# Optimization experiments

Hardware: AMD Instinct MI355X
Metric: run time of the kernel (lower is better)

Reference implementation:

```python
import jax, jax.numpy as jnp
import numpy as np

N_HEADS = 2
N_POINTS = 3
BN_EPS = 1e-5


def make_pe(C, D):
    # PositionalEncoding buffer, sliced to depth D: shape (D, C)
    pos = np.arange(D, dtype=np.float32)[:, None]
    div = np.exp(np.arange(0, C, 2, dtype=np.float32) * (-np.log(10000.0) / C))
    pe = np.zeros((D, C), dtype=np.float32)
    pe[:, 0::2] = np.sin(pos * div)
    pe[:, 1::2] = np.cos(pos * div)
    return jnp.asarray(pe)


def setup_inputs() -> dict:
    key = jax.random.key(0)
    b, c, zs, h, w = 2, 256, 32, 48, 48
    hp = N_HEADS * N_POINTS
    ks = jax.random.split(key, 8)
    features = jax.random.normal(ks[0], (b, c, zs, h, w), dtype=jnp.float32)
    # 1x1 Conv3d weights (out_ch, in_ch), no bias
    q_w = jax.random.normal(ks[1], (c, c), dtype=jnp.float32) * 0.05
    v_w = jax.random.normal(ks[2], (c, c), dtype=jnp.float32) * 0.05
    o_w = jax.random.normal(ks[3], (c, c), dtype=jnp.float32) * 0.05
    # sampling_offsets Linear: module inits weight=0, bias=[-1,-2,-3,1,2,3];
    # we add small random weight so sampling is input-dependent (non-degenerate)
    offs_w = jax.random.normal(ks[4], (hp, c), dtype=jnp.float32) * 0.02
    direction = np.array([[-1.0, -2.0, -3.0], [1.0, 2.0, 3.0]], dtype=np.float32)
    offs_b = jnp.asarray(direction.reshape(-1))
    attn_w = jax.random.normal(ks[5], (hp, c), dtype=jnp.float32) * 0.02
    attn_b = jax.random.normal(ks[6], (hp,), dtype=jnp.float32) * 0.1
    gamma = jnp.ones((c,), dtype=jnp.float32)
    beta = jnp.zeros((c,), dtype=jnp.float32)
    return {"features": features, "q_w": q_w, "v_w": v_w, "o_w": o_w,
            "offs_w": offs_w, "offs_b": offs_b, "attn_w": attn_w,
            "attn_b": attn_b, "gamma": gamma, "beta": beta}


def reference(features, q_w, v_w, o_w, offs_w, offs_b, attn_w, attn_b, gamma, beta):
    b, c, zs, h, w = features.shape
    pe = make_pe(c, zs)  # (zs, c)
    x = features + pe.T[None, :, :, None, None]  # (b,c,zs,h,w)
    # 1x1 conv3d == per-voxel channel GEMM
    q = jnp.einsum('oc,bcdhw->bodhw', q_w, x)
    v = jnp.einsum('oc,bcdhw->bodhw', v_w, x)
    # AdaptiveMaxPool1d(1) over h*w -> global spatial max; (b,zs,c)
    qp = jnp.transpose(q.max(axis=(3, 4)), (0, 2, 1))
    off = jnp.clip(qp @ offs_w.T + offs_b, 0.0, zs - 1)      # (b,zs,hp)
    attn = jax.nn.softmax(qp @ attn_w.T + attn_b, axis=-1)    # (b,zs,hp)
    lo = jnp.floor(off)
    hi = jnp.ceil(off)
    frac = off - lo
    # gather index depends only on (b,zs,hp), not (c,h,w): fold the
    # interp-weighted gather into a per-batch (zs_out, zs_in) mixing matrix.
    w_lo = attn * (1.0 - frac)
    w_hi = attn * frac
    oh_lo = jax.nn.one_hot(lo.astype(jnp.int32), zs, dtype=features.dtype)
    oh_hi = jax.nn.one_hot(hi.astype(jnp.int32), zs, dtype=features.dtype)
    M = (oh_lo * w_lo[..., None] + oh_hi * w_hi[..., None]).sum(axis=2)  # (b,zs,zs)
    samp = jnp.einsum('bzy,bcyhw->bczhw', M, v)  # (b,c,zs,h,w)
    out = jnp.einsum('oc,bcdhw->bodhw', o_w, samp)
    # BatchNorm3d, training-mode batch statistics (biased var), eps=1e-5
    mean = out.mean(axis=(0, 2, 3, 4))
    var = out.var(axis=(0, 2, 3, 4))
    normed = (out - mean[None, :, None, None, None]) * jax.lax.rsqrt(var + BN_EPS)[None, :, None, None, None]
    normed = normed * gamma[None, :, None, None, None] + beta[None, :, None, None, None]
    return normed + features
```

## Files before the change

kernel.cpp:

```cpp
#include <hip/hip_runtime.h>


#define B_   2
#define C_   256
#define Z_   32
#define HW_  2304
#define NSP  73728
#define NBN  147456.0f

typedef unsigned short u16;
typedef unsigned int   u32;
typedef __attribute__((ext_vector_type(8))) short bf16x8;
typedef __attribute__((ext_vector_type(4))) float f32x4;

__device__ int   g_isf32;
__device__ int   g_use_mfma;
__device__ float g_pe[Z_ * C_];
__device__ __align__(16) float g_wt[C_ * 512];
__device__ __align__(16) u16   g_afrag[32 * 8 * 2 * 64 * 8];
__device__ int   g_qmax[B_ * Z_ * C_];
__device__ __align__(16) float g_Mt[B_ * Z_ * Z_];
__device__ float g_bn_sum[C_];
__device__ float g_bn_ssq[C_];
__device__ float g_u[(size_t)B_ * C_ * NSP];

__device__ __forceinline__ u16 f2bf(float f) {
  u32 x = __float_as_uint(f);
  x = x + 0x7fffu + ((x >> 16) & 1u);
  return (u16)(x >> 16);
}
__device__ __forceinline__ float bf2f(u16 h) {
  return __uint_as_float(((u32)h) << 16);
}
__device__ __forceinline__ float ldx(const void* p, size_t i, int f32) {
  if (f32) return ((const float*)p)[i];
  return __uint_as_float(((u32)((const u16*)p)[i]) << 16);
}
__device__ __forceinline__ void stx(void* p, size_t i, int f32, float v) {
  if (f32) ((float*)p)[i] = v;
  else     ((u16*)p)[i] = f2bf(v);
}
__device__ __forceinline__ int f2key(float f) {
  int b = __float_as_int(f);
  return b >= 0 ? b : (b ^ 0x7fffffff);
}
__device__ __forceinline__ float key2f(int k) {
  int b = k >= 0 ? k : (k ^ 0x7fffffff);
  return __int_as_float(b);
}
__device__ __forceinline__ float sane(float v) {
  u32 a = __float_as_uint(v) & 0x7fffffffu;
  return (a >= 0x7f800000u) ? 0.f : v;
}
__device__ __forceinline__ float wredmax(float m) {
  m = fmaxf(m, __shfl_xor(m, 1));  m = fmaxf(m, __shfl_xor(m, 2));
  m = fmaxf(m, __shfl_xor(m, 4));  m = fmaxf(m, __shfl_xor(m, 8));
  m = fmaxf(m, __shfl_xor(m, 16)); m = fmaxf(m, __shfl_xor(m, 32));
  return m;
}
__device__ __forceinline__ float wredsum(float s) {
  s += __shfl_xor(s, 1);  s += __shfl_xor(s, 2);  s += __shfl_xor(s, 4);
  s += __shfl_xor(s, 8);  s += __shfl_xor(s, 16); s += __shfl_xor(s, 32);
  return s;
}


__device__ __forceinline__ void stage_x(const void* __restrict__ f, int f32,
                                        int b, int z, int ncol0, u16* xs) {
  const int tid = threadIdx.x;
  const int w = tid >> 6, l = tid & 63;
  const int n0 = (l & 15) * 4;
  const int g = l >> 4;
#pragma unroll
  for (int r = 0; r < 8; ++r) {
    const int k = r * 32 + w * 4 + g;
    const float pv = g_pe[z * C_ + k];
    const size_t fe = (size_t)(b * C_ + k) * NSP + ncol0 + n0;
    float x0, x1, x2, x3;
    if (f32) {
      const float4 v = *(const float4*)((const float*)f + fe);
      x0 = v.x; x1 = v.y; x2 = v.z; x3 = v.w;
    } else {
      x0 = ldx(f, fe + 0, 0); x1 = ldx(f, fe + 1, 0);
      x2 = ldx(f, fe + 2, 0); x3 = ldx(f, fe + 3, 0);
    }
    x0 += pv; x1 += pv; x2 += pv; x3 += pv;
#pragma unroll
    for (int e = 0; e < 4; ++e) {
      const float xv = (e == 0) ? x0 : (e == 1) ? x1 : (e == 2) ? x2 : x3;
      const int n = n0 + e;
      u32 byte = (u32)n * 512u + (u32)k * 2u;
      byte ^= (u32)(n & 15) << 4;
      xs[byte >> 1] = f2bf(xv);
    }
  }
}

__device__ __forceinline__ bf16x8 read_bfrag(const u16* xs, int j, int kk, int lane) {
  const int n = j * 16 + (lane & 15);
  u32 byte = (u32)n * 512u + (u32)kk * 64u + (u32)(lane >> 4) * 16u;
  byte ^= (u32)(n & 15) << 4;
  return *(const bf16x8*)(const void*)((const char*)xs + byte);
}

__device__ __forceinline__ bf16x8 load_afrag(int rs, int kk, int plane, int lane) {
  const size_t off = ((((size_t)(rs * 8 + kk) * 2 + plane) * 64 + lane) * 8);
  return *(const bf16x8*)(const void*)(g_afrag + off);
}

__global__ void k00_detect(const void* f) {
  const int t = threadIdx.x;
  u32 w = ((const u32*)f)[(size_t)t * 9973u];
  u32 e = (w >> 7) & 0xFFu;
  int in = (e >= 90u && e <= 140u) ? 1 : 0;
  for (int o = 1; o < 64; o <<= 1) in += __shfl_xor(in, o);
  if (t == 0) g_isf32 = (in < 40) ? 1 : 0;
}

__device__ __forceinline__ void pack_afrag(int row, int k, float val) {
  const int rs = row >> 4, kk = k >> 5, i = k & 7, g = (k >> 3) & 3;
  const int l = (row & 15) | (g << 4);
  u16 hi = f2bf(val);
  u16 lo = f2bf(val - bf2f(hi));
  const size_t u = (((size_t)(rs * 8 + kk) * 2) * 64 + l) * 8 + i;
  g_afrag[u] = hi;
  g_afrag[u + 512] = lo;
}

__global__ __launch_bounds__(256) void k0_setup(const void* o_w, const void* v_w,
                                                const void* q_w) {
  const int f32 = g_isf32;
  const int blk = blockIdx.x, t = threadIdx.x;
  if (blk < 256) {
    float acc = 0.f;
    for (int c = 0; c < 256; ++c)
      acc += ldx(o_w, (size_t)blk * 256 + c, f32) * ldx(v_w, (size_t)c * 256 + t, f32);
    g_wt[(size_t)t * 512 + blk] = acc;
    const float qv = ldx(q_w, (size_t)blk * 256 + t, f32);
    g_wt[(size_t)t * 512 + 256 + blk] = qv;
    pack_afrag(blk, t, acc);
    pack_afrag(256 + blk, t, qv);
  } else {
    const int ch = t;
    const float divf = expf(-(float)(ch >> 1) * (9.210340371976184f / 128.0f));
    for (int z = 0; z < Z_; ++z) {
      float arg = (float)z * divf;
      g_pe[z * 256 + ch] = (ch & 1) ? cosf(arg) : sinf(arg);
    }
    const int init_key = f2key(-1e30f);
    for (int k = t; k < B_ * Z_ * 256; k += 256) g_qmax[k] = init_key;
    g_bn_sum[t] = 0.f;
    g_bn_ssq[t] = 0.f;
  }
}

__global__ __launch_bounds__(512) void kP_probe(const void* __restrict__ f) {
  __shared__ u16 xs[16384];
  const int f32 = g_isf32;
  stage_x(f, f32, 0, 0, 0, xs);
  __syncthreads();
  if (threadIdx.x < 64) {
    const int lane = threadIdx.x;
    f32x4 acc = {0.f, 0.f, 0.f, 0.f};
    for (int kk = 0; kk < 8; ++kk) {
      bf16x8 bh = read_bfrag(xs, 0, kk, lane);
      bf16x8 ah = load_afrag(0, kk, 0, lane);
      bf16x8 al = load_afrag(0, kk, 1, lane);
      acc = __builtin_amdgcn_mfma_f32_16x16x32_bf16(ah, bh, acc, 0, 0, 0);
      acc = __builtin_amdgcn_mfma_f32_16x16x32_bf16(al, bh, acc, 0, 0, 0);
    }
    int ok = 1;
    const int col = lane & 15;
#pragma unroll
    for (int reg = 0; reg < 4; ++reg) {
      const int row = (lane >> 4) * 4 + reg;
      float r0 = 0.f, r1 = 0.f, r2 = 0.f, r3 = 0.f;
      for (int k = 0; k < 256; k += 4) {
        r0 = fmaf(g_wt[(size_t)(k+0) * 512 + row],
                  ldx(f, (size_t)(k+0) * NSP + col, f32) + g_pe[k+0], r0);
        r1 = fmaf(g_wt[(size_t)(k+1) * 512 + row],
                  ldx(f, (size_t)(k+1) * NSP + col, f32) + g_pe[k+1], r1);
        r2 = fmaf(g_wt[(size_t)(k+2) * 512 + row],
                  ldx(f, (size_t)(k+2) * NSP + col, f32) + g_pe[k+2], r2);
        r3 = fmaf(g_wt[(size_t)(k+3) * 512 + row],
                  ldx(f, (size_t)(k+3) * NSP + col, f32) + g_pe[k+3], r3);
      }
      float ref = (r0 + r1) + (r2 + r3);
      ok &= (fabsf(acc[reg] - ref) <= 0.02f + 0.01f * fabsf(ref)) ? 1 : 0;
    }
    ok = __all(ok);
    if (lane == 0) g_use_mfma = ok;
  }
}

__global__ __launch_bounds__(512, 4) void kA_mfma(const void* __restrict__ f) {
  if (!g_use_mfma) return;
  __shared__ u16 xs[16384];
  const int f32 = g_isf32;
  const int id = blockIdx.x;
  const int b = id / 1152;
  const int r2 = id % 1152;
  const int z = r2 / 36;
  const int m = r2 % 36;
  const int ncol0 = z * HW_ + m * 64;
  const int tid = threadIdx.x, w = tid >> 6, lane = tid & 63;

  stage_x(f, f32, b, z, ncol0, xs);
  __syncthreads();

  f32x4 acc[4][4];
  const f32x4 z4 = {0.f, 0.f, 0.f, 0.f};
#pragma unroll
  for (int r = 0; r < 4; ++r)
#pragma unroll
    for (int j = 0; j < 4; ++j) acc[r][j] = z4;

#pragma unroll 2
  for (int kk = 0; kk < 8; ++kk) {
    bf16x8 bh[4];
#pragma unroll
    for (int j = 0; j < 4; ++j) bh[j] = read_bfrag(xs, j, kk, lane);
#pragma unroll
    for (int rsl = 0; rsl < 4; ++rsl) {
      const int rs = w * 4 + rsl;
      bf16x8 ah = load_afrag(rs, kk, 0, lane);
      bf16x8 al = load_afrag(rs, kk, 1, lane);
#pragma unroll
      for (int j = 0; j < 4; ++j) {
        acc[rsl][j] = __builtin_amdgcn_mfma_f32_16x16x32_bf16(ah, bh[j], acc[rsl][j], 0, 0, 0);
        acc[rsl][j] = __builtin_amdgcn_mfma_f32_16x16x32_bf16(al, bh[j], acc[rsl][j], 0, 0, 0);
      }
    }
  }

  if (w < 4) {
#pragma unroll
    for (int rsl = 0; rsl < 4; ++rsl)
#pragma unroll
      for (int j = 0; j < 4; ++j)
#pragma unroll
        for (int reg = 0; reg < 4; ++reg) {
          const int row = (w * 4 + rsl) * 16 + (lane >> 4) * 4 + reg;
          g_u[(size_t)(b * C_ + row) * NSP + ncol0 + j * 16 + (lane & 15)] =
              acc[rsl][j][reg];
        }
  } else {
    const int rbase = (b * Z_ + z) * C_;
#pragma unroll
    for (int rsl = 0; rsl < 4; ++rsl)
#pragma unroll
      for (int reg = 0; reg < 4; ++reg) {
        float v = fmaxf(fmaxf(acc[rsl][0][reg], acc[rsl][1][reg]),
                        fmaxf(acc[rsl][2][reg], acc[rsl][3][reg]));
        v = fmaxf(v, __shfl_xor(v, 1));
        v = fmaxf(v, __shfl_xor(v, 2));
        v = fmaxf(v, __shfl_xor(v, 4));
        v = fmaxf(v, __shfl_xor(v, 8));
        if ((lane & 15) == 0)
          atomicMax(&g_qmax[rbase + ((w - 4) * 4 + rsl) * 16 + (lane >> 4) * 4 + reg],
                    f2key(v));
      }
  }
}

template<int F32>
__global__ __launch_bounds__(256) void kA_gemm(const void* __restrict__ f) {
  if (g_isf32 != F32) return;
  if (g_use_mfma) return;
  const int bid = blockIdx.x;
  const int k  = bid & 7;
  const int jj = bid >> 3;
  const int T  = k + 8 * (jj >> 3);
  const int g  = jj & 7;
  const int b  = T / 288;
  const int tz = T % 288;
  const int z  = tz / 9;
  const int hc = tz % 9;
  const int t  = threadIdx.x;
  const int n_in_z = hc * 256 + t;
  const size_t fbase = (size_t)(b * C_) * NSP + (size_t)z * HW_ + n_in_z;

  float acc[64];
#pragma unroll
  for (int i = 0; i < 64; ++i) acc[i] = 0.f;

  const float* __restrict__ wtb = g_wt + g * 64;
  const float* __restrict__ pez = g_pe + z * C_;
  for (int c = 0; c < C_; ++c) {
    float fv = ldx(f, fbase + (size_t)c * NSP, F32) + pez[c];
    const float4* __restrict__ w4 = (const float4*)(wtb + (size_t)c * 512);
#pragma unroll
    for (int q = 0; q < 16; ++q) {
      float4 wv = w4[q];
      acc[4*q+0] = fmaf(wv.x, fv, acc[4*q+0]);
      acc[4*q+1] = fmaf(wv.y, fv, acc[4*q+1]);
      acc[4*q+2] = fmaf(wv.z, fv, acc[4*q+2]);
      acc[4*q+3] = fmaf(wv.w, fv, acc[4*q+3]);
    }
  }

  if (g < 4) {
    const size_t obase = (size_t)(b * C_ + g * 64) * NSP + (size_t)z * HW_ + n_in_z;
#pragma unroll
    for (int i = 0; i < 64; ++i)
      g_u[obase + (size_t)i * NSP] = acc[i];
  } else {
    const int rbase = (b * Z_ + z) * C_ + (g - 4) * 64;
#pragma unroll
    for (int i = 0; i < 64; ++i) {
      float mres = wredmax(acc[i]);
      if ((t & 63) == 0) atomicMax(&g_qmax[rbase + i], f2key(mres));
    }
  }
}

__global__ __launch_bounds__(64) void k2_mbuild(
    const void* offs_w, const void* offs_b,
    const void* attn_w, const void* attn_b) {
  const int f32 = g_isf32;
  const int bz = blockIdx.x;
  const int lane = threadIdx.x;
  float qp[4];
#pragma unroll
  for (int i = 0; i < 4; ++i)
    qp[i] = key2f(g_qmax[bz * 256 + lane * 4 + i]);

  float res[12];
  for (int p = 0; p < 12; ++p) {
    const void* wm = (p < 6) ? offs_w : attn_w;
    const size_t row = (size_t)(p < 6 ? p : p - 6) * 256;
    float s = 0.f;
#pragma unroll
    for (int i = 0; i < 4; ++i) s += qp[i] * ldx(wm, row + lane * 4 + i, f32);
    res[p] = sane(wredsum(s));
  }

  __shared__ float sm[Z_];
  if (lane < Z_) sm[lane] = 0.f;
  __syncthreads();
  if (lane == 0) {
    float att[6], mx = -1e30f;
#pragma unroll
    for (int p = 0; p < 6; ++p) {
      att[p] = sane(res[6 + p] + ldx(attn_b, p, f32));
      mx = fmaxf(mx, att[p]);
    }
    float den = 0.f;
#pragma unroll
    for (int p = 0; p < 6; ++p) { att[p] = expf(att[p] - mx); den += att[p]; }
    float inv = 1.f / den;
#pragma unroll
    for (int p = 0; p < 6; ++p) {
      float a = att[p] * inv;
      float off = sane(res[p] + ldx(offs_b, p, f32));
      off = fminf(fmaxf(off, 0.f), 31.f);
      float lo = floorf(off), hi = ceilf(off), fr = off - lo;
      int il = min(max((int)lo, 0), 31);
      int ih = min(max((int)hi, 0), 31);
      sm[il] += a * (1.f - fr);
      sm[ih] += a * fr;
    }
  }
  __syncthreads();
  if (lane < Z_) g_Mt[((bz >> 5) * Z_ + lane) * Z_ + (bz & 31)] = sm[lane];
}

__global__ __launch_bounds__(256) void kB_mix(void* outp) {
  const int f32 = g_isf32;
  const int id = blockIdx.x;
  const int b = id / 2304;
  const int rem = id % 2304;
  const int o = rem / 9;
  const int hc = rem % 9;
  const int hw = hc * 256 + threadIdx.x;
  const size_t base = (size_t)(b * C_ + o) * NSP + hw;

  float a[Z_];
#pragma unroll
  for (int zo = 0; zo < Z_; ++zo) a[zo] = 0.f;

  for (int y = 0; y < Z_; ++y) {
    float uv = g_u[base + (size_t)y * HW_];
    const float4* __restrict__ m4 = (const float4*)(g_Mt + (size_t)(b * Z_ + y) * Z_);
#pragma unroll
    for (int q = 0; q < 8; ++q) {
      float4 mv = m4[q];
      a[4*q+0] = fmaf(mv.x, uv, a[4*q+0]);
      a[4*q+1] = fmaf(mv.y, uv, a[4*q+1]);
      a[4*q+2] = fmaf(mv.z, uv, a[4*q+2]);
      a[4*q+3] = fmaf(mv.w, uv, a[4*q+3]);
    }
  }

  float s = 0.f, ss = 0.f;
#pragma unroll
  for (int zo = 0; zo < Z_; ++zo) {
    float v = sane(a[zo]);
    stx(outp, base + (size_t)zo * HW_, f32, v);
    s += v;  ss += v * v;
  }
  s = wredsum(s);
  ss = wredsum(ss);
  if ((threadIdx.x & 63) == 0) {
    atomicAdd(&g_bn_sum[o], s);
    atomicAdd(&g_bn_ssq[o], ss);
  }
}

__global__ __launch_bounds__(256) void k5_final(
    const void* f, void* outp, const void* gamma, const void* beta) {
  const int f32 = g_isf32;
  const size_t e4 = ((size_t)blockIdx.x * 256 + threadIdx.x) * 4;
  const int o = (int)((e4 / NSP) & 255);
  const float mean = g_bn_sum[o] * (1.f / NBN);
  const float var = fmaxf(g_bn_ssq[o] * (1.f / NBN) - mean * mean, 0.f);
  const float rstd = rsqrtf(var + 1e-5f);
  const float sc = ldx(gamma, o, f32) * rstd;
  const float sh = ldx(beta, o, f32) - mean * sc;
  if (f32) {
    float4 ov = *(float4*)((float*)outp + e4);
    const float4 fv = *(const float4*)((const float*)f + e4);
    ov.x = sane(ov.x * sc + sh + fv.x);
    ov.y = sane(ov.y * sc + sh + fv.y);
    ov.z = sane(ov.z * sc + sh + fv.z);
    ov.w = sane(ov.w * sc + sh + fv.w);
    *(float4*)((float*)outp + e4) = ov;
  } else {
#pragma unroll
    for (int i = 0; i < 4; ++i) {
      float v = sane(ldx(outp, e4 + i, 0) * sc + sh + ldx(f, e4 + i, 0));
      stx(outp, e4 + i, 0, v);
    }
  }
}

extern "C" void kernel_launch(void* const* d_in, const int* in_sizes, int n_in,
                              void* d_out, int out_size, void* d_ws, size_t ws_size,
                              hipStream_t stream)
{
  (void)in_sizes; (void)n_in; (void)out_size; (void)d_ws; (void)ws_size;
  const void* f      = d_in[0];
  const void* q_w    = d_in[1];
  const void* v_w    = d_in[2];
  const void* o_w    = d_in[3];
  const void* offs_w = d_in[4];
  const void* offs_b = d_in[5];
  const void* attn_w = d_in[6];
  const void* attn_b = d_in[7];
  const void* gamma  = d_in[8];
  const void* beta   = d_in[9];

  k00_detect<<<1, 64, 0, stream>>>(f);
  k0_setup<<<257, 256, 0, stream>>>(o_w, v_w, q_w);
  kP_probe<<<1, 512, 0, stream>>>(f);
  kA_mfma<<<2304, 512, 0, stream>>>(f);
  kA_gemm<1><<<4608, 256, 0, stream>>>(f);
  kA_gemm<0><<<4608, 256, 0, stream>>>(f);
  k2_mbuild<<<64, 64, 0, stream>>>(offs_w, offs_b, attn_w, attn_b);
  kB_mix<<<4608, 256, 0, stream>>>(d_out);
  k5_final<<<36864, 256, 0, stream>>>(f, d_out, gamma, beta);
}
```

Before: 650.3 us.

## Parallelize probe check, merge fallback GEMM launches, re-tile mix kernel

The probe kernel now checks the MFMA result with 256 threads in parallel instead of serially in one wavefront, which shortens a single-block kernel on the critical path. The two templated fallback GEMM launches are merged into one runtime-dtype kernel, removing one near-empty launch. The z-mixing kernel is re-tiled so each wave handles 8 output depths for 2 adjacent columns, with float2 loads and stores and fewer accumulators per thread, at the cost of reading each u column four times across waves. The bf16 paths gain vectorized loads.

```diff
diff --git a/kernel.cpp b/kernel.cpp
--- a/kernel.cpp
+++ b/kernel.cpp
@@ -81,8 +81,8 @@
       const float4 v = *(const float4*)((const float*)f + fe);
       x0 = v.x; x1 = v.y; x2 = v.z; x3 = v.w;
     } else {
-      x0 = ldx(f, fe + 0, 0); x1 = ldx(f, fe + 1, 0);
-      x2 = ldx(f, fe + 2, 0); x3 = ldx(f, fe + 3, 0);
+      const ushort4 v = *(const ushort4*)((const u16*)f + fe);
+      x0 = bf2f(v.x); x1 = bf2f(v.y); x2 = bf2f(v.z); x3 = bf2f(v.w);
     }
     x0 += pv; x1 += pv; x2 += pv; x3 += pv;
 #pragma unroll
@@ -156,7 +156,10 @@
 
 __global__ __launch_bounds__(512) void kP_probe(const void* __restrict__ f) {
   __shared__ u16 xs[16384];
-  const int f32 = g_isf32;
+  __shared__ float smacc[64][4];
+  __shared__ int s_ok;
+  const int f32 = g_isf32;
+  if (threadIdx.x == 0) s_ok = 1;
   stage_x(f, f32, 0, 0, 0, xs);
   __syncthreads();
   if (threadIdx.x < 64) {
@@ -169,28 +172,31 @@
       acc = __builtin_amdgcn_mfma_f32_16x16x32_bf16(ah, bh, acc, 0, 0, 0);
       acc = __builtin_amdgcn_mfma_f32_16x16x32_bf16(al, bh, acc, 0, 0, 0);
     }
-    int ok = 1;
-    const int col = lane & 15;
-#pragma unroll
-    for (int reg = 0; reg < 4; ++reg) {
-      const int row = (lane >> 4) * 4 + reg;
-      float r0 = 0.f, r1 = 0.f, r2 = 0.f, r3 = 0.f;
-      for (int k = 0; k < 256; k += 4) {
-        r0 = fmaf(g_wt[(size_t)(k+0) * 512 + row],
-                  ldx(f, (size_t)(k+0) * NSP + col, f32) + g_pe[k+0], r0);
-        r1 = fmaf(g_wt[(size_t)(k+1) * 512 + row],
-                  ldx(f, (size_t)(k+1) * NSP + col, f32) + g_pe[k+1], r1);
-        r2 = fmaf(g_wt[(size_t)(k+2) * 512 + row],
-                  ldx(f, (size_t)(k+2) * NSP + col, f32) + g_pe[k+2], r2);
-        r3 = fmaf(g_wt[(size_t)(k+3) * 512 + row],
-                  ldx(f, (size_t)(k+3) * NSP + col, f32) + g_pe[k+3], r3);
-      }
-      float ref = (r0 + r1) + (r2 + r3);
-      ok &= (fabsf(acc[reg] - ref) <= 0.02f + 0.01f * fabsf(ref)) ? 1 : 0;
-    }
-    ok = __all(ok);
-    if (lane == 0) g_use_mfma = ok;
-  }
+#pragma unroll
+    for (int reg = 0; reg < 4; ++reg) smacc[lane][reg] = acc[reg];
+  }
+  __syncthreads();
+  if (threadIdx.x < 256) {
+    const int l = threadIdx.x & 63, reg = threadIdx.x >> 6;
+    const int col = l & 15;
+    const int row = (l >> 4) * 4 + reg;
+    float r0 = 0.f, r1 = 0.f, r2 = 0.f, r3 = 0.f;
+    for (int k = 0; k < 256; k += 4) {
+      r0 = fmaf(g_wt[(size_t)(k+0) * 512 + row],
+                ldx(f, (size_t)(k+0) * NSP + col, f32) + g_pe[k+0], r0);
+      r1 = fmaf(g_wt[(size_t)(k+1) * 512 + row],
+                ldx(f, (size_t)(k+1) * NSP + col, f32) + g_pe[k+1], r1);
+      r2 = fmaf(g_wt[(size_t)(k+2) * 512 + row],
+                ldx(f, (size_t)(k+2) * NSP + col, f32) + g_pe[k+2], r2);
+      r3 = fmaf(g_wt[(size_t)(k+3) * 512 + row],
+                ldx(f, (size_t)(k+3) * NSP + col, f32) + g_pe[k+3], r3);
+    }
+    float ref = (r0 + r1) + (r2 + r3);
+    if (!(fabsf(smacc[l][reg] - ref) <= 0.02f + 0.01f * fabsf(ref)))
+      atomicAnd(&s_ok, 0);
+  }
+  __syncthreads();
+  if (threadIdx.x == 0) g_use_mfma = s_ok;
 }
 
 __global__ __launch_bounds__(512, 4) void kA_mfma(const void* __restrict__ f) {
@@ -263,10 +269,9 @@
   }
 }
 
-template<int F32>
 __global__ __launch_bounds__(256) void kA_gemm(const void* __restrict__ f) {
-  if (g_isf32 != F32) return;
   if (g_use_mfma) return;
+  const int f32 = g_isf32;
   const int bid = blockIdx.x;
   const int k  = bid & 7;
   const int jj = bid >> 3;
@@ -286,8 +291,8 @@
 
   const float* __restrict__ wtb = g_wt + g * 64;
   const float* __restrict__ pez = g_pe + z * C_;
-  for (int c = 0; c < C_; ++c) {
-    float fv = ldx(f, fbase + (size_t)c * NSP, F32) + pez[c];
+  for (int c = 0; c < 256; ++c) {
+    float fv = ldx(f, fbase + (size_t)c * NSP, f32) + pez[c];
     const float4* __restrict__ w4 = (const float4*)(wtb + (size_t)c * 512);
 #pragma unroll
     for (int q = 0; q < 16; ++q) {
@@ -368,40 +373,51 @@
 __global__ __launch_bounds__(256) void kB_mix(void* outp) {
   const int f32 = g_isf32;
   const int id = blockIdx.x;
-  const int b = id / 2304;
-  const int rem = id % 2304;
-  const int o = rem / 9;
-  const int hc = rem % 9;
-  const int hw = hc * 256 + threadIdx.x;
-  const size_t base = (size_t)(b * C_ + o) * NSP + hw;
-
-  float a[Z_];
-#pragma unroll
-  for (int zo = 0; zo < Z_; ++zo) a[zo] = 0.f;
+  const int b = id / 4608;
+  const int rem = id % 4608;
+  const int o = rem / 18;
+  const int hc = rem % 18;
+  const int tid = threadIdx.x, w = tid >> 6, lane = tid & 63;
+  const int hw = hc * 128 + lane * 2;
+  const size_t ubase = (size_t)(b * C_ + o) * NSP + hw;
+  const float* __restrict__ Mtb = g_Mt + (size_t)b * Z_ * Z_ + w * 8;
+
+  float a0[8], a1[8];
+#pragma unroll
+  for (int r = 0; r < 8; ++r) { a0[r] = 0.f; a1[r] = 0.f; }
 
   for (int y = 0; y < Z_; ++y) {
-    float uv = g_u[base + (size_t)y * HW_];
-    const float4* __restrict__ m4 = (const float4*)(g_Mt + (size_t)(b * Z_ + y) * Z_);
-#pragma unroll
-    for (int q = 0; q < 8; ++q) {
-      float4 mv = m4[q];
-      a[4*q+0] = fmaf(mv.x, uv, a[4*q+0]);
-      a[4*q+1] = fmaf(mv.y, uv, a[4*q+1]);
-      a[4*q+2] = fmaf(mv.z, uv, a[4*q+2]);
-      a[4*q+3] = fmaf(mv.w, uv, a[4*q+3]);
-    }
+    const float2 uv = *(const float2*)(g_u + ubase + (size_t)y * HW_);
+    const float4 m0 = *(const float4*)(Mtb + y * Z_);
+    const float4 m1 = *(const float4*)(Mtb + y * Z_ + 4);
+    a0[0] = fmaf(m0.x, uv.x, a0[0]); a1[0] = fmaf(m0.x, uv.y, a1[0]);
+    a0[1] = fmaf(m0.y, uv.x, a0[1]); a1[1] = fmaf(m0.y, uv.y, a1[1]);
+    a0[2] = fmaf(m0.z, uv.x, a0[2]); a1[2] = fmaf(m0.z, uv.y, a1[2]);
+    a0[3] = fmaf(m0.w, uv.x, a0[3]); a1[3] = fmaf(m0.w, uv.y, a1[3]);
+    a0[4] = fmaf(m1.x, uv.x, a0[4]); a1[4] = fmaf(m1.x, uv.y, a1[4]);
+    a0[5] = fmaf(m1.y, uv.x, a0[5]); a1[5] = fmaf(m1.y, uv.y, a1[5]);
+    a0[6] = fmaf(m1.z, uv.x, a0[6]); a1[6] = fmaf(m1.z, uv.y, a1[6]);
+    a0[7] = fmaf(m1.w, uv.x, a0[7]); a1[7] = fmaf(m1.w, uv.y, a1[7]);
   }
 
   float s = 0.f, ss = 0.f;
-#pragma unroll
-  for (int zo = 0; zo < Z_; ++zo) {
-    float v = sane(a[zo]);
-    stx(outp, base + (size_t)zo * HW_, f32, v);
-    s += v;  ss += v * v;
+  const size_t obase = (size_t)(b * C_ + o) * NSP + hw;
+#pragma unroll
+  for (int r = 0; r < 8; ++r) {
+    const float v0 = sane(a0[r]);
+    const float v1 = sane(a1[r]);
+    const size_t e = obase + (size_t)(w * 8 + r) * HW_;
+    if (f32) {
+      *(float2*)((float*)outp + e) = make_float2(v0, v1);
+    } else {
+      *(u32*)((u16*)outp + e) = (u32)f2bf(v0) | ((u32)f2bf(v1) << 16);
+    }
+    s += v0 + v1;
+    ss += v0 * v0 + v1 * v1;
   }
   s = wredsum(s);
   ss = wredsum(ss);
-  if ((threadIdx.x & 63) == 0) {
+  if (lane == 0) {
     atomicAdd(&g_bn_sum[o], s);
     atomicAdd(&g_bn_ssq[o], ss);
   }
@@ -426,11 +442,14 @@
     ov.w = sane(ov.w * sc + sh + fv.w);
     *(float4*)((float*)outp + e4) = ov;
   } else {
-#pragma unroll
-    for (int i = 0; i < 4; ++i) {
-      float v = sane(ldx(outp, e4 + i, 0) * sc + sh + ldx(f, e4 + i, 0));
-      stx(outp, e4 + i, 0, v);
-    }
+    const ushort4 ov = *(const ushort4*)((const u16*)outp + e4);
+    const ushort4 fv = *(const ushort4*)((const u16*)f + e4);
+    ushort4 rv;
+    rv.x = f2bf(sane(bf2f(ov.x) * sc + sh + bf2f(fv.x)));
+    rv.y = f2bf(sane(bf2f(ov.y) * sc + sh + bf2f(fv.y)));
+    rv.z = f2bf(sane(bf2f(ov.z) * sc + sh + bf2f(fv.z)));
+    rv.w = f2bf(sane(bf2f(ov.w) * sc + sh + bf2f(fv.w)));
+    *(ushort4*)((u16*)outp + e4) = rv;
   }
 }
 
@@ -454,9 +473,8 @@
   k0_setup<<<257, 256, 0, stream>>>(o_w, v_w, q_w);
   kP_probe<<<1, 512, 0, stream>>>(f);
   kA_mfma<<<2304, 512, 0, stream>>>(f);
-  kA_gemm<1><<<4608, 256, 0, stream>>>(f);
-  kA_gemm<0><<<4608, 256, 0, stream>>>(f);
+  kA_gemm<<<4608, 256, 0, stream>>>(f);
   k2_mbuild<<<64, 64, 0, stream>>>(offs_w, offs_b, attn_w, attn_b);
-  kB_mix<<<4608, 256, 0, stream>>>(d_out);
+  kB_mix<<<9216, 256, 0, stream>>>(d_out);
   k5_final<<<36864, 256, 0, stream>>>(f, d_out, gamma, beta);
 }
```

New measurement: 706.6 us. +8.7%, slower.
